# Kernel tuning notes

Hardware: AMD Instinct MI355X
Metric: run time of the kernel (lower is better)

Reference implementation:

```python
import jax, jax.numpy as jnp
import numpy as np

B, D, U = 4096, 1024, 1024

def cumax(a):
    # Faithful to source: softmax over last axis, cumsum over axis 0 (TF defaults).
    return jnp.cumsum(jax.nn.softmax(a, axis=-1), axis=0)

def setup_inputs() -> dict:
    key = jax.random.key(0)
    ks = jax.random.split(key, 21)
    names = ['inputs', 'hidden_prev', 'cell_prev',
             'Wf', 'Uf', 'bf', 'Wi', 'Ui', 'bi', 'Wo', 'Uo', 'bo',
             'Wc', 'Uc', 'bc', 'Wft', 'Uft', 'bft', 'Wit', 'Uit', 'bit']
    shapes = [(B, D), (B, U), (B, U)] + [(D, U), (U, U), (U,)] * 6
    scales = [1.0, 1.0, 1.0] + [0.05, 0.05, 0.05] * 6  # random_normal init ~ small stddev
    return {n: jax.random.normal(k, s, dtype=jnp.float32) * sc
            for n, k, s, sc in zip(names, ks, shapes, scales)}

def reference(inputs, hidden_prev, cell_prev,
              Wf, Uf, bf, Wi, Ui, bi, Wo, Uo, bo,
              Wc, Uc, bc, Wft, Uft, bft, Wit, Uit, bit):
    # Fuse the 12 small GEMMs into 2 big ones: [B,D]@[D,6U] and [B,U]@[U,6U]
    W_all = jnp.concatenate([Wf, Wi, Wo, Wc, Wft, Wit], axis=1)   # [D, 6U]
    U_all = jnp.concatenate([Uf, Ui, Uo, Uc, Uft, Uit], axis=1)   # [U, 6U]
    b_all = jnp.concatenate([bf, bi, bo, bc, bft, bit], axis=0)   # [6U]
    pre = inputs @ W_all + hidden_prev @ U_all + b_all            # [B, 6U]
    zf, zi, zo, zc, zft, zit = [pre[:, j*U:(j+1)*U] for j in range(6)]

    f = jax.nn.sigmoid(zf)
    i = jax.nn.sigmoid(zi)
    o = jax.nn.sigmoid(zo)
    c_hat = jnp.tanh(zc)
    f_tilde = cumax(zft)
    i_tilde = 1.0 - cumax(zit)

    omega = f_tilde * i_tilde
    f_hat = f * omega + (f_tilde - omega)
    i_hat = i * omega + (i_tilde - omega)
    cell = f_hat * cell_prev + i_hat * c_hat
    hidden = o * jnp.tanh(cell)
    return hidden, cell
```

## Files before the change

### kernel.cpp

```cpp
#include <hip/hip_runtime.h>
#include <cstdint>
#include <cstddef>


typedef _Float16 half8  __attribute__((ext_vector_type(8)));
typedef _Float16 half4v __attribute__((ext_vector_type(4)));
typedef _Float16 half2v __attribute__((ext_vector_type(2)));
typedef float f32x4 __attribute__((ext_vector_type(4)));

__device__ __forceinline__ void async16(const _Float16* g, _Float16* l) {
  __builtin_amdgcn_global_load_lds(
      (const __attribute__((address_space(1))) void*)g,
      (__attribute__((address_space(3))) void*)l, 16, 0, 0);
}

struct Ptrs12 { const float* p[12]; };
struct Ptrs6  { const float* p[6];  };

__global__ void prep(const float* __restrict__ X, const float* __restrict__ H,
                     Ptrs12 w, Ptrs6 bs,
                     _Float16* __restrict__ Ahi, _Float16* __restrict__ Bhi,
                     float* __restrict__ b_all) {
  __shared__ float tile[64][65];
  const int blk = blockIdx.x;
  const int t = threadIdx.x;
  if (blk < 8192) {
    size_t base = ((size_t)blk * 256 + t) * 4;
    int k = (int)(base & 2047);
    size_t b = base >> 11;
    const float* src = (k < 1024) ? (X + b * 1024 + k) : (H + b * 1024 + (k - 1024));
    float4 v = *(const float4*)src;
    half4v hi = { (_Float16)v.x, (_Float16)v.y, (_Float16)v.z, (_Float16)v.w };
    *(half4v*)(Ahi + base) = hi;
  } else if (blk < 11264) {
    int bb = blk - 8192;
    int mat = bb >> 8;
    int tl = bb & 255;
    int tr = tl >> 4, tc = tl & 15;
    int g = mat >> 1, s = mat & 1;
    const float* src = w.p[mat];
    int col = t & 63, r0 = t >> 6;
#pragma unroll
    for (int i = 0; i < 16; i++) {
      int row = i * 4 + r0;
      tile[row][col] = src[(size_t)(tr * 64 + row) * 1024 + tc * 64 + col];
    }
    __syncthreads();
    int kh = (t & 31) * 2, r8 = t >> 5;
#pragma unroll
    for (int i = 0; i < 8; i++) {
      int c2 = i * 8 + r8;
      float v0 = tile[kh][c2] * 64.0f;
      float v1 = tile[kh + 1][c2] * 64.0f;
      size_t n  = (size_t)g * 1024 + tc * 64 + c2;
      size_t kk = (size_t)s * 1024 + tr * 64 + kh;
      *(half2v*)(Bhi + n * 2048 + kk) = half2v{ (_Float16)v0, (_Float16)v1 };
    }
  } else {
    int n = (blk - 11264) * 256 + t;
    b_all[n] = bs.p[n >> 10][n & 1023];
  }
}

__global__ __launch_bounds__(256) void gemm_split(
    const _Float16* __restrict__ Ah, const _Float16* __restrict__ Bh,
    const float* __restrict__ b_all, float* __restrict__ pre) {
  __shared__ _Float16 lds[8192];
  _Float16* sAh = lds;
  _Float16* sBh = lds + 4096;

  const int pid = blockIdx.x;
  const int group = pid / (8 * 48);
  const int rem = pid % (8 * 48);
  const int mTile = group * 8 + (rem & 7);
  const int nTile = rem >> 3;

  const int t = threadIdx.x;
  const int lane = t & 63;
  const int wave = t >> 6;
  const int waveM = wave >> 1, waveN = wave & 1;
  const int kgrp = lane >> 4, frow = lane & 15;
  const size_t baseA = (size_t)mTile * 128 * 2048;
  const size_t baseB = (size_t)nTile * 128 * 2048;

  f32x4 acc[4][4] = {};

  for (int ks = 0; ks < 64; ks++) {
    const int k0 = ks * 32;
#pragma unroll
    for (int q = 0; q < 2; q++) {
      int slot = q * 256 + t;
      int r = slot >> 2;
      int sg = slot & 3;
      int sig = sg ^ ((r >> 1) & 3);
      size_t go = (size_t)r * 2048 + k0 + sig * 8;
      async16(Ah + baseA + go, sAh + slot * 8);
      async16(Bh + baseB + go, sBh + slot * 8);
    }
    __syncthreads();

    half8 ah[4], bh[4];
#pragma unroll
    for (int mi = 0; mi < 4; mi++) {
      int r = waveM * 64 + mi * 16 + frow;
      int ps = kgrp ^ ((r >> 1) & 3);
      ah[mi] = *(const half8*)(sAh + r * 32 + ps * 8);
    }
#pragma unroll
    for (int ni = 0; ni < 4; ni++) {
      int r = waveN * 64 + ni * 16 + frow;
      int ps = kgrp ^ ((r >> 1) & 3);
      bh[ni] = *(const half8*)(sBh + r * 32 + ps * 8);
    }
#pragma unroll
    for (int mi = 0; mi < 4; mi++)
#pragma unroll
      for (int ni = 0; ni < 4; ni++)
        acc[mi][ni] = __builtin_amdgcn_mfma_f32_16x16x32_f16(ah[mi], bh[ni], acc[mi][ni], 0, 0, 0);
    __syncthreads();
  }

#pragma unroll
  for (int ni = 0; ni < 4; ni++) {
    int col = nTile * 128 + waveN * 64 + ni * 16 + frow;
    float bias = b_all[col];
#pragma unroll
    for (int mi = 0; mi < 4; mi++) {
      int rbase = mTile * 128 + waveM * 64 + mi * 16 + kgrp * 4;
#pragma unroll
      for (int j = 0; j < 4; j++)
        pre[(size_t)(rbase + j) * 6144 + col] = acc[mi][ni][j] * (1.0f / 64.0f) + bias;
    }
  }
}

__global__ void softmax_partials(float* __restrict__ pre, float* __restrict__ partials) {
  __shared__ float wsum[4][1024];
  int m = blockIdx.x >> 9;
  int ch = blockIdx.x & 511;
  int t = threadIdx.x;
  int wave = t >> 6, lane = t & 63;
  f32x4 colacc[4] = {};
  for (int rr = 0; rr < 2; rr++) {
    int b = ch * 8 + wave * 2 + rr;
    float* row = pre + (size_t)b * 6144 + (4 + m) * 1024;
    f32x4 v[4];
    float mx = -3.4e38f;
#pragma unroll
    for (int j = 0; j < 4; j++) {
      v[j] = *(const f32x4*)(row + lane * 4 + 256 * j);
      mx = fmaxf(mx, fmaxf(fmaxf(v[j][0], v[j][1]), fmaxf(v[j][2], v[j][3])));
    }
#pragma unroll
    for (int off = 32; off > 0; off >>= 1) mx = fmaxf(mx, __shfl_xor(mx, off, 64));
    float sum = 0.f;
#pragma unroll
    for (int j = 0; j < 4; j++)
#pragma unroll
      for (int q = 0; q < 4; q++) { v[j][q] = __expf(v[j][q] - mx); sum += v[j][q]; }
#pragma unroll
    for (int off = 32; off > 0; off >>= 1) sum += __shfl_xor(sum, off, 64);
    float inv = 1.f / sum;
#pragma unroll
    for (int j = 0; j < 4; j++) {
      v[j] *= inv;
      *(f32x4*)(row + lane * 4 + 256 * j) = v[j];
      colacc[j] += v[j];
    }
  }
#pragma unroll
  for (int j = 0; j < 4; j++)
    *(f32x4*)(&wsum[wave][lane * 4 + 256 * j]) = colacc[j];
  __syncthreads();
  f32x4 s = *(const f32x4*)(&wsum[0][t * 4]);
  s += *(const f32x4*)(&wsum[1][t * 4]);
  s += *(const f32x4*)(&wsum[2][t * 4]);
  s += *(const f32x4*)(&wsum[3][t * 4]);
  *(f32x4*)(partials + ((size_t)m * 512 + ch) * 1024 + t * 4) = s;
}

__global__ void scan_partials(const float* __restrict__ partials, float* __restrict__ offsets) {
  int col = blockIdx.x * 4 + (threadIdx.x >> 6);
  int lane = threadIdx.x & 63;
  int m = col >> 10, c = col & 1023;
  size_t base = (size_t)m * 512 * 1024 + c;
  float v[8];
  float s = 0.f;
#pragma unroll
  for (int j = 0; j < 8; j++) {
    v[j] = partials[base + (size_t)(lane * 8 + j) * 1024];
    s += v[j];
  }
  float incl = s;
#pragma unroll
  for (int off = 1; off < 64; off <<= 1) {
    float o = __shfl_up(incl, off, 64);
    if (lane >= off) incl += o;
  }
  float run = incl - s;
#pragma unroll
  for (int j = 0; j < 8; j++) {
    offsets[base + (size_t)(lane * 8 + j) * 1024] = run;
    run += v[j];
  }
}

__global__ void onlstm_final(const float* __restrict__ pre, const float* __restrict__ cprev,
                             const float* __restrict__ offsets, float* __restrict__ out) {
  int ch = blockIdx.x;
  int c = threadIdx.x * 4;
  f32x4 runf = *(const f32x4*)(offsets + (size_t)ch * 1024 + c);
  f32x4 runi = *(const f32x4*)(offsets + (size_t)(512 + ch) * 1024 + c);
  for (int r = 0; r < 8; r++) {
    int b = ch * 8 + r;
    const float* row = pre + (size_t)b * 6144;
    f32x4 zf = *(const f32x4*)(row + c);
    f32x4 zi = *(const f32x4*)(row + 1024 + c);
    f32x4 zo = *(const f32x4*)(row + 2048 + c);
    f32x4 zc = *(const f32x4*)(row + 3072 + c);
    f32x4 pf = *(const f32x4*)(row + 4096 + c);
    f32x4 pi = *(const f32x4*)(row + 5120 + c);
    f32x4 cp = *(const f32x4*)(cprev + (size_t)b * 1024 + c);
    runf += pf; runi += pi;
    f32x4 hid, cel;
#pragma unroll
    for (int q = 0; q < 4; q++) {
      float ft = runf[q], it = 1.f - runi[q];
      float f  = 1.f / (1.f + __expf(-zf[q]));
      float ii = 1.f / (1.f + __expf(-zi[q]));
      float o  = 1.f / (1.f + __expf(-zo[q]));
      float chat = tanhf(zc[q]);
      float omega = ft * it;
      float fhat = f * omega + (ft - omega);
      float ihat = ii * omega + (it - omega);
      float cell = fhat * cp[q] + ihat * chat;
      hid[q] = o * tanhf(cell);
      cel[q] = cell;
    }
    *(f32x4*)(out + (size_t)b * 1024 + c) = hid;
    *(f32x4*)(out + (size_t)4194304 + (size_t)b * 1024 + c) = cel;
  }
}

extern "C" void kernel_launch(void* const* d_in, const int* in_sizes, int n_in,
                              void* d_out, int out_size, void* d_ws, size_t ws_size,
                              hipStream_t stream) {
  const float* X = (const float*)d_in[0];
  const float* H = (const float*)d_in[1];
  const float* C = (const float*)d_in[2];

  char* ws = (char*)d_ws;
  float*    pre      = (float*)(ws);
  _Float16* Ahi      = (_Float16*)(ws + 100663296);
  _Float16* Bhi      = (_Float16*)(ws + 117440512);
  float*    b_all    = (float*)(ws + 142606336);
  float*    partials = (float*)(ws + 142630912);
  float*    offsets  = (float*)(ws + 146825216);

  Ptrs12 w;
  for (int g = 0; g < 6; g++) {
    w.p[2 * g]     = (const float*)d_in[3 + 3 * g];
    w.p[2 * g + 1] = (const float*)d_in[4 + 3 * g];
  }
  Ptrs6 bs;
  for (int g = 0; g < 6; g++) bs.p[g] = (const float*)d_in[5 + 3 * g];

  prep<<<11288, 256, 0, stream>>>(X, H, w, bs, Ahi, Bhi, b_all);
  gemm_split<<<1536, 256, 0, stream>>>(Ahi, Bhi, b_all, pre);
  softmax_partials<<<1024, 256, 0, stream>>>(pre, partials);
  scan_partials<<<512, 256, 0, stream>>>(partials, offsets);
  onlstm_final<<<512, 256, 0, stream>>>(pre, C, offsets, (float*)d_out);
}
```

Before: 345.8 us.

## Store gate preactivations and softmax probabilities in fp16, transpose scan partials

The GEMM epilogue now writes the four pointwise gate preactivations as fp16 into a separate buffer and keeps only the two cumax slices in fp32. The softmax kernel writes its probabilities as fp16 into a new buffer instead of overwriting in place. Per-chunk column partials are stored in a chunk-contiguous float4 layout so the scan reads them coalesced with 128 blocks. The weight-transpose prep writes 16-byte half8 stores instead of half2. Together these cut intermediate memory traffic, but fp16 rounding of the preactivations and probabilities adds error to the cumulative sums.

```diff
diff --git a/kernel.cpp b/kernel.cpp
--- a/kernel.cpp
+++ b/kernel.cpp
@@ -5,7 +5,6 @@
 
 typedef _Float16 half8  __attribute__((ext_vector_type(8)));
 typedef _Float16 half4v __attribute__((ext_vector_type(4)));
-typedef _Float16 half2v __attribute__((ext_vector_type(2)));
 typedef float f32x4 __attribute__((ext_vector_type(4)));
 
 __device__ __forceinline__ void async16(const _Float16* g, _Float16* l) {
@@ -46,16 +45,17 @@
       tile[row][col] = src[(size_t)(tr * 64 + row) * 1024 + tc * 64 + col];
     }
     __syncthreads();
-    int kh = (t & 31) * 2, r8 = t >> 5;
-#pragma unroll
-    for (int i = 0; i < 8; i++) {
-      int c2 = i * 8 + r8;
-      float v0 = tile[kh][c2] * 64.0f;
-      float v1 = tile[kh + 1][c2] * 64.0f;
-      size_t n  = (size_t)g * 1024 + tc * 64 + c2;
-      size_t kk = (size_t)s * 1024 + tr * 64 + kh;
-      *(half2v*)(Bhi + n * 2048 + kk) = half2v{ (_Float16)v0, (_Float16)v1 };
-    }
+    int c2 = t >> 2, kseg = t & 3;
+    half8 v0, v1;
+#pragma unroll
+    for (int j = 0; j < 8; j++) {
+      v0[j] = (_Float16)(tile[kseg * 16 + j][c2] * 64.0f);
+      v1[j] = (_Float16)(tile[kseg * 16 + 8 + j][c2] * 64.0f);
+    }
+    size_t n  = (size_t)g * 1024 + tc * 64 + c2;
+    size_t kk = (size_t)s * 1024 + tr * 64 + kseg * 16;
+    *(half8*)(Bhi + n * 2048 + kk) = v0;
+    *(half8*)(Bhi + n * 2048 + kk + 8) = v1;
   } else {
     int n = (blk - 11264) * 256 + t;
     b_all[n] = bs.p[n >> 10][n & 1023];
@@ -64,7 +64,8 @@
 
 __global__ __launch_bounds__(256) void gemm_split(
     const _Float16* __restrict__ Ah, const _Float16* __restrict__ Bh,
-    const float* __restrict__ b_all, float* __restrict__ pre) {
+    const float* __restrict__ b_all,
+    _Float16* __restrict__ preG, float* __restrict__ preS) {
   __shared__ _Float16 lds[8192];
   _Float16* sAh = lds;
   _Float16* sBh = lds + 4096;
@@ -120,21 +121,39 @@
     __syncthreads();
   }
 
-#pragma unroll
-  for (int ni = 0; ni < 4; ni++) {
-    int col = nTile * 128 + waveN * 64 + ni * 16 + frow;
-    float bias = b_all[col];
-#pragma unroll
-    for (int mi = 0; mi < 4; mi++) {
-      int rbase = mTile * 128 + waveM * 64 + mi * 16 + kgrp * 4;
-#pragma unroll
-      for (int j = 0; j < 4; j++)
-        pre[(size_t)(rbase + j) * 6144 + col] = acc[mi][ni][j] * (1.0f / 64.0f) + bias;
-    }
-  }
-}
-
-__global__ void softmax_partials(float* __restrict__ pre, float* __restrict__ partials) {
+  if (nTile < 32) {
+#pragma unroll
+    for (int ni = 0; ni < 4; ni++) {
+      int col = nTile * 128 + waveN * 64 + ni * 16 + frow;
+      float bias = b_all[col];
+#pragma unroll
+      for (int mi = 0; mi < 4; mi++) {
+        int rbase = mTile * 128 + waveM * 64 + mi * 16 + kgrp * 4;
+#pragma unroll
+        for (int j = 0; j < 4; j++)
+          preG[(size_t)(rbase + j) * 4096 + col] =
+              (_Float16)(acc[mi][ni][j] * (1.0f / 64.0f) + bias);
+      }
+    }
+  } else {
+#pragma unroll
+    for (int ni = 0; ni < 4; ni++) {
+      int col = (nTile - 32) * 128 + waveN * 64 + ni * 16 + frow;
+      float bias = b_all[4096 + col];
+#pragma unroll
+      for (int mi = 0; mi < 4; mi++) {
+        int rbase = mTile * 128 + waveM * 64 + mi * 16 + kgrp * 4;
+#pragma unroll
+        for (int j = 0; j < 4; j++)
+          preS[(size_t)(rbase + j) * 2048 + col] =
+              acc[mi][ni][j] * (1.0f / 64.0f) + bias;
+      }
+    }
+  }
+}
+
+__global__ void softmax_partials(const float* __restrict__ preS,
+                                 _Float16* __restrict__ P, f32x4* __restrict__ part4) {
   __shared__ float wsum[4][1024];
   int m = blockIdx.x >> 9;
   int ch = blockIdx.x & 511;
@@ -143,7 +162,8 @@
   f32x4 colacc[4] = {};
   for (int rr = 0; rr < 2; rr++) {
     int b = ch * 8 + wave * 2 + rr;
-    float* row = pre + (size_t)b * 6144 + (4 + m) * 1024;
+    const float* row = preS + (size_t)b * 2048 + m * 1024;
+    _Float16* prow = P + ((size_t)m * 4096 + b) * 1024;
     f32x4 v[4];
     float mx = -3.4e38f;
 #pragma unroll
@@ -164,7 +184,8 @@
 #pragma unroll
     for (int j = 0; j < 4; j++) {
       v[j] *= inv;
-      *(f32x4*)(row + lane * 4 + 256 * j) = v[j];
+      half4v h = { (_Float16)v[j][0], (_Float16)v[j][1], (_Float16)v[j][2], (_Float16)v[j][3] };
+      *(half4v*)(prow + lane * 4 + 256 * j) = h;
       colacc[j] += v[j];
     }
   }
@@ -176,60 +197,64 @@
   s += *(const f32x4*)(&wsum[1][t * 4]);
   s += *(const f32x4*)(&wsum[2][t * 4]);
   s += *(const f32x4*)(&wsum[3][t * 4]);
-  *(f32x4*)(partials + ((size_t)m * 512 + ch) * 1024 + t * 4) = s;
-}
-
-__global__ void scan_partials(const float* __restrict__ partials, float* __restrict__ offsets) {
-  int col = blockIdx.x * 4 + (threadIdx.x >> 6);
+  part4[((size_t)m * 256 + t) * 512 + ch] = s;
+}
+
+__global__ void scan_partials(const f32x4* __restrict__ part4, f32x4* __restrict__ off4) {
+  int gidx = blockIdx.x * 4 + (threadIdx.x >> 6);
   int lane = threadIdx.x & 63;
-  int m = col >> 10, c = col & 1023;
-  size_t base = (size_t)m * 512 * 1024 + c;
-  float v[8];
-  float s = 0.f;
+  size_t base = (size_t)gidx * 512;
+  f32x4 v[8];
+  f32x4 s = {};
 #pragma unroll
   for (int j = 0; j < 8; j++) {
-    v[j] = partials[base + (size_t)(lane * 8 + j) * 1024];
+    v[j] = part4[base + lane * 8 + j];
     s += v[j];
   }
-  float incl = s;
+  f32x4 incl = s;
 #pragma unroll
   for (int off = 1; off < 64; off <<= 1) {
-    float o = __shfl_up(incl, off, 64);
+    f32x4 o;
+#pragma unroll
+    for (int q = 0; q < 4; q++) o[q] = __shfl_up(incl[q], off, 64);
     if (lane >= off) incl += o;
   }
-  float run = incl - s;
+  f32x4 run = incl - s;
 #pragma unroll
   for (int j = 0; j < 8; j++) {
-    offsets[base + (size_t)(lane * 8 + j) * 1024] = run;
+    off4[base + lane * 8 + j] = run;
     run += v[j];
   }
 }
 
-__global__ void onlstm_final(const float* __restrict__ pre, const float* __restrict__ cprev,
-                             const float* __restrict__ offsets, float* __restrict__ out) {
+__global__ void onlstm_final(const _Float16* __restrict__ preG, const _Float16* __restrict__ P,
+                             const float* __restrict__ cprev, const f32x4* __restrict__ off4,
+                             float* __restrict__ out) {
   int ch = blockIdx.x;
-  int c = threadIdx.x * 4;
-  f32x4 runf = *(const f32x4*)(offsets + (size_t)ch * 1024 + c);
-  f32x4 runi = *(const f32x4*)(offsets + (size_t)(512 + ch) * 1024 + c);
+  int c4 = threadIdx.x;
+  int c = c4 * 4;
+  f32x4 runf = off4[(size_t)c4 * 512 + ch];
+  f32x4 runi = off4[(size_t)(256 + c4) * 512 + ch];
   for (int r = 0; r < 8; r++) {
     int b = ch * 8 + r;
-    const float* row = pre + (size_t)b * 6144;
-    f32x4 zf = *(const f32x4*)(row + c);
-    f32x4 zi = *(const f32x4*)(row + 1024 + c);
-    f32x4 zo = *(const f32x4*)(row + 2048 + c);
-    f32x4 zc = *(const f32x4*)(row + 3072 + c);
-    f32x4 pf = *(const f32x4*)(row + 4096 + c);
-    f32x4 pi = *(const f32x4*)(row + 5120 + c);
+    const _Float16* grow = preG + (size_t)b * 4096;
+    half4v zf = *(const half4v*)(grow + c);
+    half4v zi = *(const half4v*)(grow + 1024 + c);
+    half4v zo = *(const half4v*)(grow + 2048 + c);
+    half4v zc = *(const half4v*)(grow + 3072 + c);
+    half4v pf = *(const half4v*)(P + (size_t)b * 1024 + c);
+    half4v pi = *(const half4v*)(P + (size_t)(4096 + b) * 1024 + c);
     f32x4 cp = *(const f32x4*)(cprev + (size_t)b * 1024 + c);
-    runf += pf; runi += pi;
     f32x4 hid, cel;
 #pragma unroll
     for (int q = 0; q < 4; q++) {
+      runf[q] += (float)pf[q];
+      runi[q] += (float)pi[q];
       float ft = runf[q], it = 1.f - runi[q];
-      float f  = 1.f / (1.f + __expf(-zf[q]));
-      float ii = 1.f / (1.f + __expf(-zi[q]));
-      float o  = 1.f / (1.f + __expf(-zo[q]));
-      float chat = tanhf(zc[q]);
+      float f  = 1.f / (1.f + __expf(-(float)zf[q]));
+      float ii = 1.f / (1.f + __expf(-(float)zi[q]));
+      float o  = 1.f / (1.f + __expf(-(float)zo[q]));
+      float chat = tanhf((float)zc[q]);
       float omega = ft * it;
       float fhat = f * omega + (ft - omega);
       float ihat = ii * omega + (it - omega);
@@ -250,12 +275,14 @@
   const float* C = (const float*)d_in[2];
 
   char* ws = (char*)d_ws;
-  float*    pre      = (float*)(ws);
-  _Float16* Ahi      = (_Float16*)(ws + 100663296);
-  _Float16* Bhi      = (_Float16*)(ws + 117440512);
-  float*    b_all    = (float*)(ws + 142606336);
-  float*    partials = (float*)(ws + 142630912);
-  float*    offsets  = (float*)(ws + 146825216);
+  _Float16* preG  = (_Float16*)(ws);
+  float*    preS  = (float*)(ws + 33554432);
+  _Float16* Ahi   = (_Float16*)(ws + 67108864);
+  _Float16* Bhi   = (_Float16*)(ws + 83886080);
+  _Float16* P     = (_Float16*)(ws + 109051904);
+  float*    b_all = (float*)(ws + 125829120);
+  f32x4*    part4 = (f32x4*)(ws + 125853696);
+  f32x4*    off4  = (f32x4*)(ws + 130048000);
 
   Ptrs12 w;
   for (int g = 0; g < 6; g++) {
@@ -266,8 +293,8 @@
   for (int g = 0; g < 6; g++) bs.p[g] = (const float*)d_in[5 + 3 * g];
 
   prep<<<11288, 256, 0, stream>>>(X, H, w, bs, Ahi, Bhi, b_all);
-  gemm_split<<<1536, 256, 0, stream>>>(Ahi, Bhi, b_all, pre);
-  softmax_partials<<<1024, 256, 0, stream>>>(pre, partials);
-  scan_partials<<<512, 256, 0, stream>>>(partials, offsets);
-  onlstm_final<<<512, 256, 0, stream>>>(pre, C, offsets, (float*)d_out);
-}
+  gemm_split<<<1536, 256, 0, stream>>>(Ahi, Bhi, b_all, preG, preS);
+  softmax_partials<<<1024, 256, 0, stream>>>(preS, P, part4);
+  scan_partials<<<128, 256, 0, stream>>>(part4, off4);
+  onlstm_final<<<512, 256, 0, stream>>>(preG, P, C, off4, (float*)d_out);
+}
```

After: 344.8 us. Within noise of the previous version (-0.3%).
